# Kernel optimization log

Hardware: AMD Instinct MI355X
Metric: run time of the kernel (lower is better)

## Reference

```python
import jax, jax.numpy as jnp
import numpy as np

B, T, H, LD, FFN, TED = 4, 4096, 8, 128, 512, 2048
D = H * LD
LN_EPS = 1e-5


def setup_inputs() -> dict:
    key = jax.random.key(0)
    ks = jax.random.split(key, 8)
    s = lambda k, shape, sc=0.02: jax.random.normal(k, shape, jnp.float32) * sc
    return dict(
        x=s(ks[0], (B, T, D), 1.0),
        emb=s(ks[1], (B, TED), 1.0),
        W1=s(ks[2], (H, LD, FFN)),   # per-head linear1 weights
        b1=jnp.zeros((H, FFN), jnp.float32),
        W2=s(ks[3], (H, FFN, LD)),   # per-head linear2 weights
        b2=jnp.zeros((H, LD), jnp.float32),
        ln_w=jnp.ones((D,), jnp.float32),
        ln_b=jnp.zeros((D,), jnp.float32),
        emb_W=s(ks[4], (TED, 2 * D)),
        emb_b=jnp.zeros((2 * D,), jnp.float32),
        out_W=s(ks[5], (D, D)),
        out_b=jnp.zeros((D,), jnp.float32),
    )


def reference(x, emb, W1, b1, W2, b2, ln_w, ln_b, emb_W, emb_b, out_W, out_b):
    Bx, Tx, Dx = x.shape
    Hx = W1.shape[0]
    xh = x.reshape(Bx, Tx, Hx, -1)                      # (B,T,H,ld)
    # batched per-head 2-layer MLP (replaces the Python loop over heads)
    h1 = jax.nn.gelu(jnp.einsum('bthd,hdf->bthf', xh, W1) + b1, approximate=False)
    y = jnp.einsum('bthf,hfd->bthd', h1, W2) + b2       # (B,T,H,ld)
    y = y.reshape(Bx, Tx, Dx)                            # concat over heads
    # StylizationBlock: SiLU -> Linear -> scale/shift; LN modulate; SiLU -> Linear
    emb_out = jax.nn.silu(emb) @ emb_W + emb_b           # (B, 2D)
    scale, shift = jnp.split(emb_out[:, None, :], 2, axis=-1)
    mu = jnp.mean(y, axis=-1, keepdims=True)
    var = jnp.var(y, axis=-1, keepdims=True)
    yn = (y - mu) * jax.lax.rsqrt(var + LN_EPS) * ln_w + ln_b
    h = yn * (1.0 + scale) + shift
    out = jax.nn.silu(h) @ out_W + out_b
    return x + out
```

## Files before the change

### kernel.cpp

```cpp
#include <hip/hip_runtime.h>
#include <hip/hip_bf16.h>
#include <math.h>

#define B_     4
#define T_     4096
#define H_     8
#define LD_    128
#define FFN_   512
#define D_     1024
#define TED_   2048
#define TWO_D_ 2048
#define NTOK_  (B_ * T_)
#define LN_EPS_ 1e-5f

#define WS_EMB_OFF   0
#define WS_IMG1_OFF  (64 * 1024)
#define WS_IMG2_OFF  ((64 << 10) + (1 << 20))
#define WS_IMGO_OFF  ((64 << 10) + (2 << 20))
#define WS_Y_OFF     (8 << 20)

typedef short bf16x8 __attribute__((ext_vector_type(8)));
typedef float f32x4  __attribute__((ext_vector_type(4)));
typedef float f32x16 __attribute__((ext_vector_type(16)));
typedef unsigned int u32x4 __attribute__((ext_vector_type(4)));

__device__ __forceinline__ float siluf(float v) {
  return v * __builtin_amdgcn_rcpf(1.0f + __expf(-v));
}
__device__ __forceinline__ float geluf(float v) {
  const float s  = v * 0.70710678118654752440f;
  const float ax = fabsf(s);
  const float t  = __builtin_amdgcn_rcpf(fmaf(0.3275911f, ax, 1.0f));
  const float e  = __expf(-ax * ax);
  float p = fmaf(1.061405429f, t, -1.453152027f);
  p = fmaf(p, t, 1.421413741f);
  p = fmaf(p, t, -0.284496736f);
  p = fmaf(p, t, 0.254829592f);
  p = p * t;
  const float erf_ax = fmaf(-p, e, 1.0f);
  const float erf_s  = copysignf(erf_ax, s);
  return 0.5f * v * (1.0f + erf_s);
}
__device__ __forceinline__ unsigned short f2bf(float v) {
  unsigned int u = __float_as_uint(v);
  u += 0x7fffu + ((u >> 16) & 1u);
  return (unsigned short)(u >> 16);
}
__device__ __forceinline__ unsigned int pack2(float a, float b) {
  unsigned int r;
  asm("v_cvt_pk_bf16_f32 %0, %1, %2" : "=v"(r) : "v"(a), "v"(b));
  return r;
}
__device__ __forceinline__ void unpack8(uint4 u, float* v) {
  v[0] = __uint_as_float(u.x << 16); v[1] = __uint_as_float(u.x & 0xffff0000u);
  v[2] = __uint_as_float(u.y << 16); v[3] = __uint_as_float(u.y & 0xffff0000u);
  v[4] = __uint_as_float(u.z << 16); v[5] = __uint_as_float(u.z & 0xffff0000u);
  v[6] = __uint_as_float(u.w << 16); v[7] = __uint_as_float(u.w & 0xffff0000u);
}

__device__ __forceinline__ void gload_lds16(const void* g, void* l) {
#pragma clang diagnostic push
#pragma clang diagnostic ignored "-Waddress-space-conversion"
  __builtin_amdgcn_global_load_lds(
      (const __attribute__((address_space(1))) unsigned int*)g,
      (__attribute__((address_space(3))) unsigned int*)l, 16, 0, 0);
#pragma clang diagnostic pop
}

__global__ __launch_bounds__(256) void kinit(
    const float* __restrict__ W1, const float* __restrict__ W2,
    const float* __restrict__ out_W,
    const float* __restrict__ emb, const float* __restrict__ emb_W,
    const float* __restrict__ emb_b,
    unsigned short* __restrict__ img1, unsigned short* __restrict__ img2,
    unsigned short* __restrict__ imgO, float* __restrict__ emb_out) {
  const int t = blockIdx.x;
  const int tid = threadIdx.x;
  if (t < 64) {
    const bool is1 = (t < 32);
    const int h = (t & 31) >> 2, q = t & 3;
    const int l = tid & 63, fg = tid >> 6;
    const int l31 = l & 31, hi8 = (l >> 5) * 8;
    #pragma unroll
    for (int i = 0; i < 8; ++i) {
      const int fid = fg * 8 + i;
      float val[8];
      size_t dsto;
      if (is1) {
        const int c = q * 4 + (fid >> 3), kb = fid & 7;
        const float* sp = W1 + (size_t)h * 65536 +
                          (size_t)(kb * 16 + hi8) * 512 + c * 32 + l31;
        #pragma unroll
        for (int j = 0; j < 8; ++j) val[j] = sp[(size_t)j * 512];
        dsto = (size_t)h * 65536 + (size_t)(c * 8 + kb) * 512 + l * 8;
      } else {
        const int c = q * 4 + (fid >> 3), kb2 = (fid >> 2) & 1, nt = fid & 3;
        const float* sp = W2 + (size_t)h * 65536 +
                          (size_t)(c * 32 + kb2 * 16 + hi8) * 128 + nt * 32 + l31;
        #pragma unroll
        for (int j = 0; j < 8; ++j) val[j] = sp[(size_t)j * 128];
        dsto = (size_t)h * 65536 + (size_t)(c * 8 + kb2 * 4 + nt) * 512 + l * 8;
      }
      unsigned int p[4];
      #pragma unroll
      for (int qq = 0; qq < 4; ++qq) p[qq] = pack2(val[2 * qq], val[2 * qq + 1]);
      *reinterpret_cast<uint4*>((is1 ? img1 : img2) + dsto) =
          make_uint4(p[0], p[1], p[2], p[3]);
    }
    return;
  }
  if (t < 128) {
    __shared__ float ls[128][129];
    const int tt = t - 64, tr = tt >> 3, tc = tt & 7;
    const float* src = out_W + (size_t)tr * 128 * 1024 + tc * 128;
    unsigned short* dst = imgO + (size_t)tc * 128 * 1024 + tr * 128;
    for (int i = tid; i < 128 * 32; i += 256) {
      const int r = i >> 5, c4 = (i & 31) << 2;
      const float4 v = *reinterpret_cast<const float4*>(src + (size_t)r * 1024 + c4);
      ls[r][c4] = v.x; ls[r][c4 + 1] = v.y; ls[r][c4 + 2] = v.z; ls[r][c4 + 3] = v.w;
    }
    __syncthreads();
    for (int u = tid; u < 2048; u += 256) {
      const int nn = u >> 4, kb = (u & 15) << 3;
      unsigned int p[4];
      #pragma unroll
      for (int qq = 0; qq < 4; ++qq)
        p[qq] = pack2(ls[kb + 2 * qq][nn], ls[kb + 2 * qq + 1][nn]);
      *reinterpret_cast<uint4*>(dst + (size_t)nn * 1024 + kb) =
          make_uint4(p[0], p[1], p[2], p[3]);
    }
    return;
  }
  {
    __shared__ float se[B_][128];
    const int bid = t - 128;
    const int j   = (bid & 7) * 256 + tid;
    const int k0  = (bid >> 3) * 128;
    for (int i = tid; i < B_ * 128; i += 256) {
      const int b = i >> 7, k = i & 127;
      se[b][k] = siluf(emb[b * TED_ + k0 + k]);
    }
    __syncthreads();
    float a0 = 0.f, a1 = 0.f, a2 = 0.f, a3 = 0.f;
    const float* Wp = emb_W + (size_t)k0 * TWO_D_ + j;
    for (int k = 0; k < 128; ++k) {
      const float w = Wp[(size_t)k * TWO_D_];
      a0 += se[0][k] * w; a1 += se[1][k] * w;
      a2 += se[2][k] * w; a3 += se[3][k] * w;
    }
    if ((bid >> 3) == 0) {
      const float bb = emb_b[j];
      a0 += bb; a1 += bb; a2 += bb; a3 += bb;
    }
    atomicAdd(&emb_out[0 * TWO_D_ + j], a0);
    atomicAdd(&emb_out[1 * TWO_D_ + j], a1);
    atomicAdd(&emb_out[2 * TWO_D_ + j], a2);
    atomicAdd(&emb_out[3 * TWO_D_ + j], a3);
  }
}

__global__ __launch_bounds__(256, 3) void k1_mfma(
    const float* __restrict__ x,
    const unsigned short* __restrict__ img1,
    const unsigned short* __restrict__ img2,
    const float* __restrict__ b1, const float* __restrict__ b2,
    unsigned short* __restrict__ y) {
  __shared__ unsigned short wbuf[2][16 * 512];
  const int h = blockIdx.y;
  const int tid = threadIdx.x, w = tid >> 6, l = tid & 63;
  const int t0 = blockIdx.x * 128 + w * 32;
  const int l31 = l & 31, hi = l >> 5;

  const unsigned short* s1 = img1 + ((size_t)h << 16);
  const unsigned short* s2 = img2 + ((size_t)h << 16);

  auto stage = [&](unsigned short* buf, int c) {
    #pragma unroll
    for (int i = 0; i < 4; ++i) {
      const int slot = w * 4 + i;
      const unsigned short* src = (slot < 8)
          ? (s1 + (size_t)(c * 8 + slot) * 512 + l * 8)
          : (s2 + (size_t)(c * 8 + (slot - 8)) * 512 + l * 8);
      gload_lds16(src, buf + slot * 512);
    }
  };

  bf16x8 xf[8];
  {
    const float* xr = x + (size_t)(t0 + l31) * D_ + h * LD_ + hi * 8;
    #pragma unroll
    for (int kb = 0; kb < 8; ++kb) {
      const float4 a = *reinterpret_cast<const float4*>(xr + kb * 16);
      const float4 b = *reinterpret_cast<const float4*>(xr + kb * 16 + 4);
      u32x4 u;
      u[0] = pack2(a.x, a.y); u[1] = pack2(a.z, a.w);
      u[2] = pack2(b.x, b.y); u[3] = pack2(b.z, b.w);
      xf[kb] = __builtin_bit_cast(bf16x8, u);
    }
  }

  f32x16 acc2[4];
  #pragma unroll
  for (int nt = 0; nt < 4; ++nt)
    #pragma unroll
    for (int r = 0; r < 16; ++r) acc2[nt][r] = 0.f;

  auto compute = [&](const unsigned short* buf, int c) {
    f32x16 acc1;
    #pragma unroll
    for (int r = 0; r < 16; ++r) acc1[r] = 0.f;
    __builtin_amdgcn_s_setprio(1);
    #pragma unroll
    for (int kb = 0; kb < 8; ++kb) {
      const bf16x8 a = *reinterpret_cast<const bf16x8*>(buf + kb * 512 + l * 8);
      acc1 = __builtin_amdgcn_mfma_f32_32x32x16_bf16(a, xf[kb], acc1, 0, 0, 0);
    }
    __builtin_amdgcn_s_setprio(0);
    float g[16];
    #pragma unroll
    for (int q = 0; q < 4; ++q) {
      const float4 bq = *reinterpret_cast<const float4*>(
          b1 + h * FFN_ + c * 32 + q * 8 + hi * 4);
      g[q*4+0] = geluf(acc1[q*4+0] + bq.x);
      g[q*4+1] = geluf(acc1[q*4+1] + bq.y);
      g[q*4+2] = geluf(acc1[q*4+2] + bq.z);
      g[q*4+3] = geluf(acc1[q*4+3] + bq.w);
    }
    unsigned int P[4][2];
    #pragma unroll
    for (int q = 0; q < 4; ++q) {
      P[q][0] = pack2(g[q*4+0], g[q*4+1]);
      P[q][1] = pack2(g[q*4+2], g[q*4+3]);
    }
    unsigned int A2[2][4];
    #pragma unroll
    for (int half = 0; half < 2; ++half) {
      const int qe = half * 2, qo = half * 2 + 1;
      #pragma unroll
      for (int s = 0; s < 2; ++s) {
        const unsigned int offer = hi ? P[qe][s] : P[qo][s];
        const unsigned int recv =
            (unsigned int)__shfl_xor((int)offer, 32);
        A2[half][s]     = hi ? recv : P[qe][s];
        A2[half][s + 2] = hi ? P[qo][s] : recv;
      }
    }
    __builtin_amdgcn_s_setprio(1);
    #pragma unroll
    for (int kb2 = 0; kb2 < 2; ++kb2) {
      u32x4 t;
      t[0] = A2[kb2][0]; t[1] = A2[kb2][1];
      t[2] = A2[kb2][2]; t[3] = A2[kb2][3];
      const bf16x8 a2 = __builtin_bit_cast(bf16x8, t);
      #pragma unroll
      for (int nt = 0; nt < 4; ++nt) {
        const bf16x8 b2f = *reinterpret_cast<const bf16x8*>(
            buf + (8 + kb2 * 4 + nt) * 512 + l * 8);
        acc2[nt] = __builtin_amdgcn_mfma_f32_32x32x16_bf16(a2, b2f, acc2[nt], 0, 0, 0);
      }
    }
    __builtin_amdgcn_s_setprio(0);
  };

  stage(wbuf[0], 0);
  __syncthreads();
  #pragma unroll 1
  for (int c = 0; c < 16; c += 2) {
    if (c + 1 < 16) stage(wbuf[1], c + 1);
    compute(wbuf[0], c);
    __syncthreads();
    if (c + 2 < 16) stage(wbuf[0], c + 2);
    compute(wbuf[1], c + 1);
    __syncthreads();
  }

  #pragma unroll
  for (int nt = 0; nt < 4; ++nt) {
    const int d = nt * 32 + l31;
    const float bb = b2[h * LD_ + d];
    #pragma unroll
    for (int rp = 0; rp < 8; ++rp) {
      const int r0 = 2 * rp, r1 = 2 * rp + 1;
      const unsigned int pk = pack2(acc2[nt][r0] + bb, acc2[nt][r1] + bb);
      const int tA = t0 + (r0 & 3) + 8 * (r0 >> 2) + 4 * hi;
      const int tB = tA + 1;
      y[(size_t)tA * D_ + h * LD_ + d] = (unsigned short)(pk & 0xffffu);
      y[(size_t)tB * D_ + h * LD_ + d] = (unsigned short)(pk >> 16);
    }
  }
}

__global__ __launch_bounds__(256) void k2_ln(
    unsigned short* __restrict__ y, const float* __restrict__ ln_w,
    const float* __restrict__ ln_b, const float* __restrict__ emb_out) {
  const int tid = threadIdx.x;
  const int bt  = blockIdx.x * 4 + (tid >> 6);
  const int l   = tid & 63;
  const int b   = bt >> 12;
  unsigned short* rowp = y + (size_t)bt * D_ + l * 16;
  const uint4 u0 = *reinterpret_cast<const uint4*>(rowp);
  const uint4 u1 = *reinterpret_cast<const uint4*>(rowp + 8);
  float v[16];
  unpack8(u0, v); unpack8(u1, v + 8);
  float s = 0.f, s2 = 0.f;
  #pragma unroll
  for (int j = 0; j < 16; ++j) { s += v[j]; s2 += v[j] * v[j]; }
  #pragma unroll
  for (int off = 1; off < 64; off <<= 1) {
    s  += __shfl_xor(s, off);
    s2 += __shfl_xor(s2, off);
  }
  const float mu   = s * (1.0f / D_);
  const float rstd = rsqrtf(s2 * (1.0f / D_) - mu * mu + LN_EPS_);
  const int d0 = l * 16;
  float r[16];
  #pragma unroll
  for (int q = 0; q < 4; ++q) {
    const float4 lw = *reinterpret_cast<const float4*>(ln_w + d0 + q * 4);
    const float4 lb = *reinterpret_cast<const float4*>(ln_b + d0 + q * 4);
    const float4 sc = *reinterpret_cast<const float4*>(emb_out + (size_t)b * TWO_D_ + d0 + q * 4);
    const float4 sh = *reinterpret_cast<const float4*>(emb_out + (size_t)b * TWO_D_ + D_ + d0 + q * 4);
    r[q*4+0] = siluf(((v[q*4+0] - mu) * rstd * lw.x + lb.x) * (1.f + sc.x) + sh.x);
    r[q*4+1] = siluf(((v[q*4+1] - mu) * rstd * lw.y + lb.y) * (1.f + sc.y) + sh.y);
    r[q*4+2] = siluf(((v[q*4+2] - mu) * rstd * lw.z + lb.z) * (1.f + sc.z) + sh.z);
    r[q*4+3] = siluf(((v[q*4+3] - mu) * rstd * lw.w + lb.w) * (1.f + sc.w) + sh.w);
  }
  uint4 o0, o1;
  o0.x = pack2(r[0], r[1]);  o0.y = pack2(r[2], r[3]);
  o0.z = pack2(r[4], r[5]);  o0.w = pack2(r[6], r[7]);
  o1.x = pack2(r[8], r[9]);  o1.y = pack2(r[10], r[11]);
  o1.z = pack2(r[12], r[13]); o1.w = pack2(r[14], r[15]);
  *reinterpret_cast<uint4*>(rowp)     = o0;
  *reinterpret_cast<uint4*>(rowp + 8) = o1;
}

__global__ __launch_bounds__(512) void k3_mfma(
    const unsigned short* __restrict__ hb,
    const unsigned short* __restrict__ imgO,
    const float* __restrict__ out_b, const float* __restrict__ x,
    float* __restrict__ out) {
  __shared__ unsigned short As[2][256 * 64];
  __shared__ unsigned short Bs[2][256 * 64];
  const int bid = blockIdx.x;
  const int swz = (bid & 7) * 32 + (bid >> 3);
  const int m0 = (swz >> 2) * 256;
  const int n0 = (swz & 3) * 256;
  const int tid = threadIdx.x, w = tid >> 6, l = tid & 63;
  const int lr = l & 15, lg = l >> 4;
  const int wr = (w >> 2) * 128;
  const int wc = (w & 3) * 64;

  f32x4 acc[8][4];
  #pragma unroll
  for (int mf = 0; mf < 8; ++mf)
    #pragma unroll
    for (int nf = 0; nf < 4; ++nf)
      acc[mf][nf] = (f32x4){0.f, 0.f, 0.f, 0.f};

  const int grl  = l >> 3;
  const int gcol = (((l & 7) ^ ((l >> 3) & 7)) * 8);

  auto stage = [&](int kt, int b) {
    #pragma unroll
    for (int j = 0; j < 4; ++j) {
      const int slab = j * 8 + w;
      const int row = slab * 8 + grl;
      gload_lds16(hb   + (size_t)(m0 + row) * D_ + kt * 64 + gcol,
                  &As[b][slab * 512]);
      gload_lds16(imgO + (size_t)(n0 + row) * D_ + kt * 64 + gcol,
                  &Bs[b][slab * 512]);
    }
  };

  auto compute = [&](int b) {
    #pragma unroll
    for (int ks = 0; ks < 2; ++ks) {
      bf16x8 af[8], bf[4];
      #pragma unroll
      for (int mf = 0; mf < 8; ++mf) {
        const int row = wr + mf * 16 + lr;
        const int u = (ks * 4 + lg) ^ (row & 7);
        af[mf] = *reinterpret_cast<const bf16x8*>(&As[b][row * 64 + u * 8]);
      }
      #pragma unroll
      for (int nf = 0; nf < 4; ++nf) {
        const int row = wc + nf * 16 + lr;
        const int u = (ks * 4 + lg) ^ (row & 7);
        bf[nf] = *reinterpret_cast<const bf16x8*>(&Bs[b][row * 64 + u * 8]);
      }
      #pragma unroll
      for (int mf = 0; mf < 8; ++mf)
        #pragma unroll
        for (int nf = 0; nf < 4; ++nf)
          acc[mf][nf] = __builtin_amdgcn_mfma_f32_16x16x32_bf16(
              af[mf], bf[nf], acc[mf][nf], 0, 0, 0);
    }
  };

  stage(0, 0);
  __syncthreads();
  #pragma unroll 1
  for (int kt = 0; kt < 16; ++kt) {
    const int cur = kt & 1;
    if (kt + 1 < 16) stage(kt + 1, cur ^ 1);
    compute(cur);
    __syncthreads();
  }

  #pragma unroll
  for (int mf = 0; mf < 8; ++mf) {
    #pragma unroll
    for (int nf = 0; nf < 4; ++nf) {
      const int n = n0 + wc + nf * 16 + lr;
      const float bb = out_b[n];
      #pragma unroll
      for (int r = 0; r < 4; ++r) {
        const int m = m0 + wr + mf * 16 + lg * 4 + r;
        out[(size_t)m * D_ + n] = acc[mf][nf][r] + bb + x[(size_t)m * D_ + n];
      }
    }
  }
}

extern "C" void kernel_launch(void* const* d_in, const int* in_sizes, int n_in,
                              void* d_out, int out_size, void* d_ws, size_t ws_size,
                              hipStream_t stream) {
  const float* x     = (const float*)d_in[0];
  const float* emb   = (const float*)d_in[1];
  const float* W1    = (const float*)d_in[2];
  const float* b1    = (const float*)d_in[3];
  const float* W2    = (const float*)d_in[4];
  const float* b2    = (const float*)d_in[5];
  const float* ln_w  = (const float*)d_in[6];
  const float* ln_b  = (const float*)d_in[7];
  const float* emb_W = (const float*)d_in[8];
  const float* emb_b = (const float*)d_in[9];
  const float* out_W = (const float*)d_in[10];
  const float* out_b = (const float*)d_in[11];
  float* out = (float*)d_out;

  float*          emb_out = (float*)((char*)d_ws + WS_EMB_OFF);
  unsigned short* img1    = (unsigned short*)((char*)d_ws + WS_IMG1_OFF);
  unsigned short* img2    = (unsigned short*)((char*)d_ws + WS_IMG2_OFF);
  unsigned short* imgO    = (unsigned short*)((char*)d_ws + WS_IMGO_OFF);
  unsigned short* ybuf    = (unsigned short*)((char*)d_ws + WS_Y_OFF);

  hipMemsetAsync(emb_out, 0, B_ * TWO_D_ * sizeof(float), stream);
  kinit<<<256, 256, 0, stream>>>(W1, W2, out_W, emb, emb_W, emb_b,
                                 img1, img2, imgO, emb_out);
  k1_mfma<<<dim3(NTOK_ / 128, H_), 256, 0, stream>>>(x, img1, img2, b1, b2, ybuf);
  k2_ln<<<NTOK_ / 4, 256, 0, stream>>>(ybuf, ln_w, ln_b, emb_out);
  k3_mfma<<<256, 512, 0, stream>>>(ybuf, imgO, out_b, x, out);
}
```

Measured before the change: 161.5 us.

## Switch per-head MLP kernel from 32x32 to 16x16x32 MFMA tiles

Rewrites the per-head MLP kernel to use 16x16x32 bf16 MFMA instructions with 16 tokens per wave instead of 32. The weight-image layout produced by the init kernel and the lane shuffles that turn GELU outputs into the second GEMM's operand are redone to match. Blocks now cover 64 tokens, the grid doubles, and launch bounds allow 4 blocks per CU for more occupancy. The cost is that each block stages the full weight chunks for half as many tokens, which halves weight reuse from LDS and doubles the total weight traffic.

```diff
diff --git a/kernel.cpp b/kernel.cpp
--- a/kernel.cpp
+++ b/kernel.cpp
@@ -21,7 +21,6 @@
 
 typedef short bf16x8 __attribute__((ext_vector_type(8)));
 typedef float f32x4  __attribute__((ext_vector_type(4)));
-typedef float f32x16 __attribute__((ext_vector_type(16)));
 typedef unsigned int u32x4 __attribute__((ext_vector_type(4)));
 
 __device__ __forceinline__ float siluf(float v) {
@@ -41,11 +40,6 @@
   const float erf_s  = copysignf(erf_ax, s);
   return 0.5f * v * (1.0f + erf_s);
 }
-__device__ __forceinline__ unsigned short f2bf(float v) {
-  unsigned int u = __float_as_uint(v);
-  u += 0x7fffu + ((u >> 16) & 1u);
-  return (unsigned short)(u >> 16);
-}
 __device__ __forceinline__ unsigned int pack2(float a, float b) {
   unsigned int r;
   asm("v_cvt_pk_bf16_f32 %0, %1, %2" : "=v"(r) : "v"(a), "v"(b));
@@ -78,28 +72,29 @@
   const int tid = threadIdx.x;
   if (t < 64) {
     const bool is1 = (t < 32);
-    const int h = (t & 31) >> 2, q = t & 3;
+    const int h = (t & 31) >> 2, q4 = t & 3;
     const int l = tid & 63, fg = tid >> 6;
-    const int l31 = l & 31, hi8 = (l >> 5) * 8;
+    const int m15 = l & 15, qj = ((l >> 4) & 3) * 8;
     #pragma unroll
     for (int i = 0; i < 8; ++i) {
       const int fid = fg * 8 + i;
+      const int c   = q4 * 4 + (fid >> 3);
+      const int sub = fid & 7;
       float val[8];
-      size_t dsto;
+      const size_t dsto =
+          (size_t)h * 65536 + (size_t)(c * 8 + sub) * 512 + l * 8;
       if (is1) {
-        const int c = q * 4 + (fid >> 3), kb = fid & 7;
+        const int fh = sub >> 2, kb = sub & 3;
         const float* sp = W1 + (size_t)h * 65536 +
-                          (size_t)(kb * 16 + hi8) * 512 + c * 32 + l31;
+                          (size_t)(kb * 32 + qj) * 512 + c * 32 + fh * 16 + m15;
         #pragma unroll
         for (int j = 0; j < 8; ++j) val[j] = sp[(size_t)j * 512];
-        dsto = (size_t)h * 65536 + (size_t)(c * 8 + kb) * 512 + l * 8;
       } else {
-        const int c = q * 4 + (fid >> 3), kb2 = (fid >> 2) & 1, nt = fid & 3;
+        const int nt = sub;
         const float* sp = W2 + (size_t)h * 65536 +
-                          (size_t)(c * 32 + kb2 * 16 + hi8) * 128 + nt * 32 + l31;
+                          (size_t)(c * 32 + qj) * 128 + nt * 16 + m15;
         #pragma unroll
         for (int j = 0; j < 8; ++j) val[j] = sp[(size_t)j * 128];
-        dsto = (size_t)h * 65536 + (size_t)(c * 8 + kb2 * 4 + nt) * 512 + l * 8;
       }
       unsigned int p[4];
       #pragma unroll
@@ -159,7 +154,7 @@
   }
 }
 
-__global__ __launch_bounds__(256, 3) void k1_mfma(
+__global__ __launch_bounds__(256, 4) void k1_mfma(
     const float* __restrict__ x,
     const unsigned short* __restrict__ img1,
     const unsigned short* __restrict__ img2,
@@ -168,8 +163,8 @@
   __shared__ unsigned short wbuf[2][16 * 512];
   const int h = blockIdx.y;
   const int tid = threadIdx.x, w = tid >> 6, l = tid & 63;
-  const int t0 = blockIdx.x * 128 + w * 32;
-  const int l31 = l & 31, hi = l >> 5;
+  const int t0 = blockIdx.x * 64 + w * 16;
+  const int m15 = l & 15, q = l >> 4, qj = q * 8;
 
   const unsigned short* s1 = img1 + ((size_t)h << 16);
   const unsigned short* s2 = img2 + ((size_t)h << 16);
@@ -185,13 +180,13 @@
     }
   };
 
-  bf16x8 xf[8];
+  bf16x8 xf[4];
   {
-    const float* xr = x + (size_t)(t0 + l31) * D_ + h * LD_ + hi * 8;
-    #pragma unroll
-    for (int kb = 0; kb < 8; ++kb) {
-      const float4 a = *reinterpret_cast<const float4*>(xr + kb * 16);
-      const float4 b = *reinterpret_cast<const float4*>(xr + kb * 16 + 4);
+    const float* xr = x + (size_t)(t0 + m15) * D_ + h * LD_ + qj;
+    #pragma unroll
+    for (int kb = 0; kb < 4; ++kb) {
+      const float4 a = *reinterpret_cast<const float4*>(xr + kb * 32);
+      const float4 b = *reinterpret_cast<const float4*>(xr + kb * 32 + 4);
       u32x4 u;
       u[0] = pack2(a.x, a.y); u[1] = pack2(a.z, a.w);
       u[2] = pack2(b.x, b.y); u[3] = pack2(b.z, b.w);
@@ -199,65 +194,53 @@
     }
   }
 
-  f32x16 acc2[4];
-  #pragma unroll
-  for (int nt = 0; nt < 4; ++nt)
-    #pragma unroll
-    for (int r = 0; r < 16; ++r) acc2[nt][r] = 0.f;
+  f32x4 acc2[8];
+  #pragma unroll
+  for (int nt = 0; nt < 8; ++nt) acc2[nt] = (f32x4){0.f, 0.f, 0.f, 0.f};
 
   auto compute = [&](const unsigned short* buf, int c) {
-    f32x16 acc1;
-    #pragma unroll
-    for (int r = 0; r < 16; ++r) acc1[r] = 0.f;
+    f32x4 acc1h[2];
+    acc1h[0] = (f32x4){0.f, 0.f, 0.f, 0.f};
+    acc1h[1] = (f32x4){0.f, 0.f, 0.f, 0.f};
     __builtin_amdgcn_s_setprio(1);
     #pragma unroll
-    for (int kb = 0; kb < 8; ++kb) {
-      const bf16x8 a = *reinterpret_cast<const bf16x8*>(buf + kb * 512 + l * 8);
-      acc1 = __builtin_amdgcn_mfma_f32_32x32x16_bf16(a, xf[kb], acc1, 0, 0, 0);
-    }
+    for (int fh = 0; fh < 2; ++fh)
+      #pragma unroll
+      for (int kb = 0; kb < 4; ++kb) {
+        const bf16x8 a = *reinterpret_cast<const bf16x8*>(
+            buf + (fh * 4 + kb) * 512 + l * 8);
+        acc1h[fh] = __builtin_amdgcn_mfma_f32_16x16x32_bf16(a, xf[kb], acc1h[fh], 0, 0, 0);
+      }
     __builtin_amdgcn_s_setprio(0);
-    float g[16];
-    #pragma unroll
-    for (int q = 0; q < 4; ++q) {
+    unsigned int P[2][2];
+    #pragma unroll
+    for (int fh = 0; fh < 2; ++fh) {
       const float4 bq = *reinterpret_cast<const float4*>(
-          b1 + h * FFN_ + c * 32 + q * 8 + hi * 4);
-      g[q*4+0] = geluf(acc1[q*4+0] + bq.x);
-      g[q*4+1] = geluf(acc1[q*4+1] + bq.y);
-      g[q*4+2] = geluf(acc1[q*4+2] + bq.z);
-      g[q*4+3] = geluf(acc1[q*4+3] + bq.w);
-    }
-    unsigned int P[4][2];
-    #pragma unroll
-    for (int q = 0; q < 4; ++q) {
-      P[q][0] = pack2(g[q*4+0], g[q*4+1]);
-      P[q][1] = pack2(g[q*4+2], g[q*4+3]);
-    }
-    unsigned int A2[2][4];
-    #pragma unroll
-    for (int half = 0; half < 2; ++half) {
-      const int qe = half * 2, qo = half * 2 + 1;
-      #pragma unroll
-      for (int s = 0; s < 2; ++s) {
-        const unsigned int offer = hi ? P[qe][s] : P[qo][s];
-        const unsigned int recv =
-            (unsigned int)__shfl_xor((int)offer, 32);
-        A2[half][s]     = hi ? recv : P[qe][s];
-        A2[half][s + 2] = hi ? P[qo][s] : recv;
-      }
-    }
+          b1 + h * FFN_ + c * 32 + fh * 16 + q * 4);
+      const float g0 = geluf(acc1h[fh][0] + bq.x);
+      const float g1 = geluf(acc1h[fh][1] + bq.y);
+      const float g2 = geluf(acc1h[fh][2] + bq.z);
+      const float g3 = geluf(acc1h[fh][3] + bq.w);
+      P[fh][0] = pack2(g0, g1);
+      P[fh][1] = pack2(g2, g3);
+    }
+    unsigned int A2[4];
+    #pragma unroll
+    for (int k = 0; k < 4; ++k) {
+      const int srcLane = (2 * (q & 1) + (k >> 1)) * 16 + m15;
+      const unsigned int v0 = (unsigned int)__shfl((int)P[0][k & 1], srcLane);
+      const unsigned int v1 = (unsigned int)__shfl((int)P[1][k & 1], srcLane);
+      A2[k] = (q >> 1) ? v1 : v0;
+    }
+    u32x4 tt;
+    tt[0] = A2[0]; tt[1] = A2[1]; tt[2] = A2[2]; tt[3] = A2[3];
+    const bf16x8 a2 = __builtin_bit_cast(bf16x8, tt);
     __builtin_amdgcn_s_setprio(1);
     #pragma unroll
-    for (int kb2 = 0; kb2 < 2; ++kb2) {
-      u32x4 t;
-      t[0] = A2[kb2][0]; t[1] = A2[kb2][1];
-      t[2] = A2[kb2][2]; t[3] = A2[kb2][3];
-      const bf16x8 a2 = __builtin_bit_cast(bf16x8, t);
-      #pragma unroll
-      for (int nt = 0; nt < 4; ++nt) {
-        const bf16x8 b2f = *reinterpret_cast<const bf16x8*>(
-            buf + (8 + kb2 * 4 + nt) * 512 + l * 8);
-        acc2[nt] = __builtin_amdgcn_mfma_f32_32x32x16_bf16(a2, b2f, acc2[nt], 0, 0, 0);
-      }
+    for (int nt = 0; nt < 8; ++nt) {
+      const bf16x8 b2f = *reinterpret_cast<const bf16x8*>(
+          buf + (8 + nt) * 512 + l * 8);
+      acc2[nt] = __builtin_amdgcn_mfma_f32_16x16x32_bf16(a2, b2f, acc2[nt], 0, 0, 0);
     }
     __builtin_amdgcn_s_setprio(0);
   };
@@ -275,17 +258,16 @@
   }
 
   #pragma unroll
-  for (int nt = 0; nt < 4; ++nt) {
-    const int d = nt * 32 + l31;
+  for (int nt = 0; nt < 8; ++nt) {
+    const int d = nt * 16 + m15;
     const float bb = b2[h * LD_ + d];
     #pragma unroll
-    for (int rp = 0; rp < 8; ++rp) {
-      const int r0 = 2 * rp, r1 = 2 * rp + 1;
-      const unsigned int pk = pack2(acc2[nt][r0] + bb, acc2[nt][r1] + bb);
-      const int tA = t0 + (r0 & 3) + 8 * (r0 >> 2) + 4 * hi;
-      const int tB = tA + 1;
-      y[(size_t)tA * D_ + h * LD_ + d] = (unsigned short)(pk & 0xffffu);
-      y[(size_t)tB * D_ + h * LD_ + d] = (unsigned short)(pk >> 16);
+    for (int rp = 0; rp < 2; ++rp) {
+      const unsigned int pk =
+          pack2(acc2[nt][2 * rp] + bb, acc2[nt][2 * rp + 1] + bb);
+      const int tA = t0 + q * 4 + 2 * rp;
+      y[(size_t)tA * D_ + h * LD_ + d]       = (unsigned short)(pk & 0xffffu);
+      y[(size_t)(tA + 1) * D_ + h * LD_ + d] = (unsigned short)(pk >> 16);
     }
   }
 }
@@ -448,7 +430,7 @@
   hipMemsetAsync(emb_out, 0, B_ * TWO_D_ * sizeof(float), stream);
   kinit<<<256, 256, 0, stream>>>(W1, W2, out_W, emb, emb_W, emb_b,
                                  img1, img2, imgO, emb_out);
-  k1_mfma<<<dim3(NTOK_ / 128, H_), 256, 0, stream>>>(x, img1, img2, b1, b2, ybuf);
+  k1_mfma<<<dim3(NTOK_ / 64, H_), 256, 0, stream>>>(x, img1, img2, b1, b2, ybuf);
   k2_ln<<<NTOK_ / 4, 256, 0, stream>>>(ybuf, ln_w, ln_b, emb_out);
   k3_mfma<<<256, 512, 0, stream>>>(ybuf, imgO, out_b, x, out);
 }
```

Measured after the change: 163.8 us. Within noise of the previous version (+1.4%).

## Fuse LayerNorm modulation and SiLU into the output GEMM's A-operand load

Applied to the files above, without the earlier changes.

Removes the separate LN kernel. The output GEMM now computes per-row mean/rstd from the raw y rows in a prologue and precomputes the combined LN-weight/scale and bias/shift vectors into shared memory. It then applies the normalization, modulation and SiLU to A fragments after loading them from LDS, before the MFMAs. This avoids a full write and reread of the intermediate activation and one launch. In exchange, it repeats the stats pass and the transcendental work for each column block, and adds VALU work inside the MFMA loop, plus setprio hints around the MFMAs.

```diff
diff --git a/kernel.cpp b/kernel.cpp
--- a/kernel.cpp
+++ b/kernel.cpp
@@ -40,11 +40,6 @@
   const float erf_ax = fmaf(-p, e, 1.0f);
   const float erf_s  = copysignf(erf_ax, s);
   return 0.5f * v * (1.0f + erf_s);
-}
-__device__ __forceinline__ unsigned short f2bf(float v) {
-  unsigned int u = __float_as_uint(v);
-  u += 0x7fffu + ((u >> 16) & 1u);
-  return (unsigned short)(u >> 16);
 }
 __device__ __forceinline__ unsigned int pack2(float a, float b) {
   unsigned int r;
@@ -290,61 +285,23 @@
   }
 }
 
-__global__ __launch_bounds__(256) void k2_ln(
-    unsigned short* __restrict__ y, const float* __restrict__ ln_w,
-    const float* __restrict__ ln_b, const float* __restrict__ emb_out) {
-  const int tid = threadIdx.x;
-  const int bt  = blockIdx.x * 4 + (tid >> 6);
-  const int l   = tid & 63;
-  const int b   = bt >> 12;
-  unsigned short* rowp = y + (size_t)bt * D_ + l * 16;
-  const uint4 u0 = *reinterpret_cast<const uint4*>(rowp);
-  const uint4 u1 = *reinterpret_cast<const uint4*>(rowp + 8);
-  float v[16];
-  unpack8(u0, v); unpack8(u1, v + 8);
-  float s = 0.f, s2 = 0.f;
-  #pragma unroll
-  for (int j = 0; j < 16; ++j) { s += v[j]; s2 += v[j] * v[j]; }
-  #pragma unroll
-  for (int off = 1; off < 64; off <<= 1) {
-    s  += __shfl_xor(s, off);
-    s2 += __shfl_xor(s2, off);
-  }
-  const float mu   = s * (1.0f / D_);
-  const float rstd = rsqrtf(s2 * (1.0f / D_) - mu * mu + LN_EPS_);
-  const int d0 = l * 16;
-  float r[16];
-  #pragma unroll
-  for (int q = 0; q < 4; ++q) {
-    const float4 lw = *reinterpret_cast<const float4*>(ln_w + d0 + q * 4);
-    const float4 lb = *reinterpret_cast<const float4*>(ln_b + d0 + q * 4);
-    const float4 sc = *reinterpret_cast<const float4*>(emb_out + (size_t)b * TWO_D_ + d0 + q * 4);
-    const float4 sh = *reinterpret_cast<const float4*>(emb_out + (size_t)b * TWO_D_ + D_ + d0 + q * 4);
-    r[q*4+0] = siluf(((v[q*4+0] - mu) * rstd * lw.x + lb.x) * (1.f + sc.x) + sh.x);
-    r[q*4+1] = siluf(((v[q*4+1] - mu) * rstd * lw.y + lb.y) * (1.f + sc.y) + sh.y);
-    r[q*4+2] = siluf(((v[q*4+2] - mu) * rstd * lw.z + lb.z) * (1.f + sc.z) + sh.z);
-    r[q*4+3] = siluf(((v[q*4+3] - mu) * rstd * lw.w + lb.w) * (1.f + sc.w) + sh.w);
-  }
-  uint4 o0, o1;
-  o0.x = pack2(r[0], r[1]);  o0.y = pack2(r[2], r[3]);
-  o0.z = pack2(r[4], r[5]);  o0.w = pack2(r[6], r[7]);
-  o1.x = pack2(r[8], r[9]);  o1.y = pack2(r[10], r[11]);
-  o1.z = pack2(r[12], r[13]); o1.w = pack2(r[14], r[15]);
-  *reinterpret_cast<uint4*>(rowp)     = o0;
-  *reinterpret_cast<uint4*>(rowp + 8) = o1;
-}
-
-__global__ __launch_bounds__(512) void k3_mfma(
-    const unsigned short* __restrict__ hb,
+__global__ __launch_bounds__(512, 1) void k3f(
+    const unsigned short* __restrict__ yb,
     const unsigned short* __restrict__ imgO,
     const float* __restrict__ out_b, const float* __restrict__ x,
-    float* __restrict__ out) {
+    const float* __restrict__ ln_w, const float* __restrict__ ln_b,
+    const float* __restrict__ emb_out, float* __restrict__ out) {
   __shared__ unsigned short As[2][256 * 64];
   __shared__ unsigned short Bs[2][256 * 64];
+  __shared__ float murs_s[256];
+  __shared__ float rstd_s[256];
+  __shared__ float lwsc_s[1024];
+  __shared__ float lbs_s[1024];
   const int bid = blockIdx.x;
   const int swz = (bid & 7) * 32 + (bid >> 3);
   const int m0 = (swz >> 2) * 256;
   const int n0 = (swz & 3) * 256;
+  const int b  = m0 >> 12;
   const int tid = threadIdx.x, w = tid >> 6, l = tid & 63;
   const int lr = l & 15, lg = l >> 4;
   const int wr = (w >> 2) * 128;
@@ -360,50 +317,130 @@
   const int grl  = l >> 3;
   const int gcol = (((l & 7) ^ ((l >> 3) & 7)) * 8);
 
-  auto stage = [&](int kt, int b) {
+  auto stage = [&](int kt, int bb) {
     #pragma unroll
     for (int j = 0; j < 4; ++j) {
       const int slab = j * 8 + w;
       const int row = slab * 8 + grl;
-      gload_lds16(hb   + (size_t)(m0 + row) * D_ + kt * 64 + gcol,
-                  &As[b][slab * 512]);
+      gload_lds16(yb   + (size_t)(m0 + row) * D_ + kt * 64 + gcol,
+                  &As[bb][slab * 512]);
       gload_lds16(imgO + (size_t)(n0 + row) * D_ + kt * 64 + gcol,
-                  &Bs[b][slab * 512]);
+                  &Bs[bb][slab * 512]);
     }
   };
 
-  auto compute = [&](int b) {
+  stage(0, 0);
+
+  {
+    #pragma unroll 1
+    for (int i = 0; i < 32; ++i) {
+      const int row = w * 32 + i;
+      const unsigned short* rp = yb + (size_t)(m0 + row) * D_ + l * 16;
+      const uint4 u0 = *reinterpret_cast<const uint4*>(rp);
+      const uint4 u1 = *reinterpret_cast<const uint4*>(rp + 8);
+      float v[16];
+      unpack8(u0, v); unpack8(u1, v + 8);
+      float s = 0.f, s2 = 0.f;
+      #pragma unroll
+      for (int j = 0; j < 16; ++j) { s += v[j]; s2 += v[j] * v[j]; }
+      #pragma unroll
+      for (int off = 1; off < 64; off <<= 1) {
+        s  += __shfl_xor(s, off);
+        s2 += __shfl_xor(s2, off);
+      }
+      if (l == 0) {
+        const float mu   = s * (1.0f / D_);
+        const float rstd = rsqrtf(s2 * (1.0f / D_) - mu * mu + LN_EPS_);
+        murs_s[row] = mu * rstd;
+        rstd_s[row] = rstd;
+      }
+    }
+  }
+  {
+    #pragma unroll
+    for (int e = 0; e < 2; ++e) {
+      const int c = tid * 2 + e;
+      const float sc = emb_out[(size_t)b * TWO_D_ + c];
+      const float sh = emb_out[(size_t)b * TWO_D_ + D_ + c];
+      const float os = 1.0f + sc;
+      lwsc_s[c] = ln_w[c] * os;
+      lbs_s[c]  = fmaf(ln_b[c], os, sh);
+    }
+  }
+  __syncthreads();
+
+  float murs8[8], rstd8[8];
+  #pragma unroll
+  for (int mf = 0; mf < 8; ++mf) {
+    const int row = wr + mf * 16 + lr;
+    murs8[mf] = murs_s[row];
+    rstd8[mf] = rstd_s[row];
+  }
+
+  auto compute = [&](int bb, int kt) {
     #pragma unroll
     for (int ks = 0; ks < 2; ++ks) {
+      const int colu = ks * 4 + lg;
+      const float* lwp = &lwsc_s[kt * 64 + colu * 8];
+      const float* lbp = &lbs_s[kt * 64 + colu * 8];
+      float lwv[8], lbv[8];
+      {
+        const float4 a0 = *reinterpret_cast<const float4*>(lwp);
+        const float4 a1 = *reinterpret_cast<const float4*>(lwp + 4);
+        const float4 c0 = *reinterpret_cast<const float4*>(lbp);
+        const float4 c1 = *reinterpret_cast<const float4*>(lbp + 4);
+        lwv[0]=a0.x; lwv[1]=a0.y; lwv[2]=a0.z; lwv[3]=a0.w;
+        lwv[4]=a1.x; lwv[5]=a1.y; lwv[6]=a1.z; lwv[7]=a1.w;
+        lbv[0]=c0.x; lbv[1]=c0.y; lbv[2]=c0.z; lbv[3]=c0.w;
+        lbv[4]=c1.x; lbv[5]=c1.y; lbv[6]=c1.z; lbv[7]=c1.w;
+      }
       bf16x8 af[8], bf[4];
       #pragma unroll
       for (int mf = 0; mf < 8; ++mf) {
         const int row = wr + mf * 16 + lr;
-        const int u = (ks * 4 + lg) ^ (row & 7);
-        af[mf] = *reinterpret_cast<const bf16x8*>(&As[b][row * 64 + u * 8]);
+        const int u = colu ^ (row & 7);
+        const bf16x8 raw = *reinterpret_cast<const bf16x8*>(
+            &As[bb][row * 64 + u * 8]);
+        float vv[8];
+        unpack8(__builtin_bit_cast(uint4, raw), vv);
+        unsigned int pk[4];
+        #pragma unroll
+        for (int j2 = 0; j2 < 4; ++j2) {
+          float o2[2];
+          #pragma unroll
+          for (int e = 0; e < 2; ++e) {
+            const int j = j2 * 2 + e;
+            const float tl = fmaf(vv[j], rstd8[mf] * lwv[j],
+                                  fmaf(-murs8[mf], lwv[j], lbv[j]));
+            o2[e] = siluf(tl);
+          }
+          pk[j2] = pack2(o2[0], o2[1]);
+        }
+        af[mf] = __builtin_bit_cast(bf16x8,
+                                    make_uint4(pk[0], pk[1], pk[2], pk[3]));
       }
       #pragma unroll
       for (int nf = 0; nf < 4; ++nf) {
         const int row = wc + nf * 16 + lr;
-        const int u = (ks * 4 + lg) ^ (row & 7);
-        bf[nf] = *reinterpret_cast<const bf16x8*>(&Bs[b][row * 64 + u * 8]);
-      }
+        const int u = colu ^ (row & 7);
+        bf[nf] = *reinterpret_cast<const bf16x8*>(&Bs[bb][row * 64 + u * 8]);
+      }
+      __builtin_amdgcn_s_setprio(1);
       #pragma unroll
       for (int mf = 0; mf < 8; ++mf)
         #pragma unroll
         for (int nf = 0; nf < 4; ++nf)
           acc[mf][nf] = __builtin_amdgcn_mfma_f32_16x16x32_bf16(
               af[mf], bf[nf], acc[mf][nf], 0, 0, 0);
+      __builtin_amdgcn_s_setprio(0);
     }
   };
 
-  stage(0, 0);
-  __syncthreads();
   #pragma unroll 1
   for (int kt = 0; kt < 16; ++kt) {
     const int cur = kt & 1;
     if (kt + 1 < 16) stage(kt + 1, cur ^ 1);
-    compute(cur);
+    compute(cur, kt);
     __syncthreads();
   }
 
@@ -449,6 +486,5 @@
   kinit<<<256, 256, 0, stream>>>(W1, W2, out_W, emb, emb_W, emb_b,
                                  img1, img2, imgO, emb_out);
   k1_mfma<<<dim3(NTOK_ / 128, H_), 256, 0, stream>>>(x, img1, img2, b1, b2, ybuf);
-  k2_ln<<<NTOK_ / 4, 256, 0, stream>>>(ybuf, ln_w, ln_b, emb_out);
-  k3_mfma<<<256, 512, 0, stream>>>(ybuf, imgO, out_b, x, out);
-}
+  k3f<<<256, 512, 0, stream>>>(ybuf, imgO, out_b, x, ln_w, ln_b, emb_out, out);
+}
```

Result: slower. 233.0 us (+44.3%).
